# Performance work log

Measured on AMD Instinct MI355X. Metric: run time of the kernel, lower is better.

Reference implementation:

```python
import jax, jax.numpy as jnp
import numpy as np

K = 16  # memory_topk

def signed_abs_softmax(x, axis=-1):
    # sign(x) * softmax(|x|): the module's 'signed_abs_softmax' route/edge compression
    return jnp.sign(x) * jax.nn.softmax(jnp.abs(x), axis=axis)

def unit_norm(v, eps=1e-6):
    return v / (jnp.linalg.norm(v, axis=-1, keepdims=True) + eps)

def setup_inputs() -> dict:
    key = jax.random.key(0)
    ks = jax.random.split(key, 7)
    B, T, D, S, R = 8, 2048, 512, 2048, 64
    std = 0.02
    return {
        "x": jax.random.normal(ks[0], (B, T, D), jnp.float32),
        "init_state": std * jax.random.normal(ks[1], (S,), jnp.float32),
        "init_val": std * jax.random.normal(ks[2], (S, D), jnp.float32),
        "route_a": std * jax.random.normal(ks[3], (D, R), jnp.float32),
        "route_b": std * jax.random.normal(ks[4], (R, S), jnp.float32),
        "pair_a": std * jax.random.normal(ks[5], (D, R), jnp.float32),
        "pair_b": std * jax.random.normal(ks[6], (D, R), jnp.float32),
    }

def reference(x, init_state, init_val, route_a, route_b, pair_a, pair_b):
    B, T, D = x.shape
    S = init_val.shape[0]
    b_idx = jnp.arange(B)[:, None, None]

    # --- initialize memory level (signed-softmax state, unit-norm values) ---
    state = jnp.broadcast_to(signed_abs_softmax(init_state), (B, S))
    val = jnp.broadcast_to(unit_norm(init_val), (B, S, D))

    # --- SparseTransition write: topk route tokens -> slots, scatter-add ---
    scores = jnp.einsum('btd,dr,rs->bts', x, route_a, route_b)   # [B,T,S] low-rank route
    _, idx = jax.lax.top_k(jnp.abs(scores), K)                    # [B,T,K] topk by magnitude
    g = jnp.take_along_axis(scores, idx, axis=-1)                 # signed gathered scores
    w = signed_abs_softmax(g, axis=-1)                            # route compression
    v = unit_norm(x)                                              # use_direction_only=True
    val_delta = jnp.zeros((B, S, D), x.dtype).at[b_idx, idx].add(w[..., None] * v[:, :, None, :])
    state_delta = jnp.zeros((B, S), x.dtype).at[b_idx, idx].add(jax.nn.softplus(g))
    state = signed_abs_softmax(state + state_delta, axis=-1)      # merge='add' + signed softmax state
    val = unit_norm(val + val_delta)                              # merge='add' + unit-norm values

    # --- SparsePropagation: topk pairwise edges among slots, residual mix ---
    q = jnp.einsum('bsd,dr->bsr', val, pair_a)
    kk = jnp.einsum('bsd,dr->bsr', val, pair_b)
    p = jnp.einsum('bir,bjr->bij', q, kk)                         # [B,S,S] low-rank pairwise
    _, eidx = jax.lax.top_k(jnp.abs(p), K)                        # [B,S,K] topk edges per slot
    pe = jnp.take_along_axis(p, eidx, axis=-1)
    ew = signed_abs_softmax(pe, axis=-1)                          # edge compression
    nbr = val[b_idx, eidx]                                        # [B,S,K,D] gather neighbor values
    delta = jnp.einsum('bsk,bskd->bsd', ew, nbr)
    val = unit_norm(val + delta)                                  # residual + unit-norm

    # pack (state, val) into one array: [B,S,1+D]
    return jnp.concatenate([state[..., None], val], axis=-1)
```

## Files before the change

### kernel.cpp

```cpp
#include <hip/hip_runtime.h>
#include <cmath>

namespace {
constexpr int B = 8;
constexpr int T = 2048;
constexpr int D = 512;
constexpr int S = 2048;
constexpr int R = 64;
constexpr int KTOP = 16;
constexpr int NT = 8;
constexpr int NR = 16;
constexpr int NI = 8;
constexpr int CAP = 256;

__device__ __forceinline__ float signf(float v) {
    return (v > 0.f) ? 1.f : ((v < 0.f) ? -1.f : 0.f);
}

__device__ __forceinline__ void topk16_row(float* __restrict__ row,
                                           unsigned long long* __restrict__ cand,
                                           int lane, float& myg, int& myj) {
    const float4* p4 = (const float4*)row;
    float lmax = 0.f;
#pragma unroll
    for (int i = 0; i < 8; i++) {
        float4 v = p4[lane + 64 * i];
        lmax = fmaxf(lmax, fmaxf(fmaxf(fabsf(v.x), fabsf(v.y)),
                                 fmaxf(fabsf(v.z), fabsf(v.w))));
    }
    {
        float v = lmax;
#pragma unroll
        for (int size = 2; size <= 64; size <<= 1) {
#pragma unroll
            for (int stride = size >> 1; stride > 0; stride >>= 1) {
                float o = __shfl_xor(v, stride, 64);
                bool takeMax = ((lane & size) == 0) == ((lane & stride) == 0);
                v = takeMax ? fmaxf(v, o) : fminf(v, o);
            }
        }
        lmax = __shfl(v, 15);
    }
    float t = lmax;
    int cnt = 0;
#pragma unroll
    for (int i = 0; i < 8; i++) {
        float4 v = p4[lane + 64 * i];
        cnt += (fabsf(v.x) >= t) + (fabsf(v.y) >= t) +
               (fabsf(v.z) >= t) + (fabsf(v.w) >= t);
    }
    int off = cnt;
#pragma unroll
    for (int d = 1; d < 64; d <<= 1) {
        int o = __shfl_up(off, d, 64);
        if (lane >= d) off += o;
    }
    int total = __shfl(off, 63);
    int base = off - cnt;

    if (total <= 64) {
        int pos = base;
#pragma unroll
        for (int i = 0; i < 8; i++) {
            float4 v = p4[lane + 64 * i];
            int jb = 4 * (lane + 64 * i);
            float c[4] = {v.x, v.y, v.z, v.w};
#pragma unroll
            for (int cc = 0; cc < 4; cc++) {
                if (fabsf(c[cc]) >= t) {
                    unsigned ab = __float_as_uint(c[cc]) & 0x7fffffffu;
                    cand[pos++] = ((unsigned long long)ab << 11) |
                                  (unsigned)(2047 - (jb + cc));
                }
            }
        }
        unsigned long long key = (lane < total) ? cand[lane] : 0ull;
#pragma unroll
        for (int size = 2; size <= 64; size <<= 1) {
#pragma unroll
            for (int stride = size >> 1; stride > 0; stride >>= 1) {
                unsigned long long o = __shfl_xor((long long)key, stride, 64);
                bool takeMax = ((lane & size) == 0) == ((lane & stride) == 0);
                key = (takeMax == (key > o)) ? key : o;
            }
        }
        myg = 0.f; myj = 0;
        if (lane < KTOP) {
            myj = 2047 - (int)(key & 2047ull);
            myg = row[myj];
        }
    } else {
        myg = 0.f; myj = 0;
        for (int k = 0; k < KTOP; k++) {
            float bv = -1.f, bs = 0.f; int bj = 0;
#pragma unroll
            for (int i = 0; i < 8; i++) {
                float4 v = p4[lane + 64 * i];
                int jb = 4 * (lane + 64 * i);
                { float a = fabsf(v.x); if (a > bv) { bv = a; bs = v.x; bj = jb; } }
                { float a = fabsf(v.y); if (a > bv) { bv = a; bs = v.y; bj = jb + 1; } }
                { float a = fabsf(v.z); if (a > bv) { bv = a; bs = v.z; bj = jb + 2; } }
                { float a = fabsf(v.w); if (a > bv) { bv = a; bs = v.w; bj = jb + 3; } }
            }
#pragma unroll
            for (int off2 = 32; off2 > 0; off2 >>= 1) {
                float ov = __shfl_xor(bv, off2, 64);
                float os = __shfl_xor(bs, off2, 64);
                int   oj = __shfl_xor(bj, off2, 64);
                if (ov > bv || (ov == bv && oj < bj)) { bv = ov; bs = os; bj = oj; }
            }
            if (lane == k) { myg = bs; myj = bj; }
            if (lane == 0) row[bj] = 0.f;
        }
    }
}
}

__global__ void k_init_state(const float* __restrict__ init_state,
                             float* __restrict__ state_ws) {
    int b = blockIdx.x;
    int tid = threadIdx.x;
    __shared__ float red[256];
    float m = -1e30f;
    for (int s = tid; s < S; s += 256) m = fmaxf(m, fabsf(init_state[s]));
    red[tid] = m; __syncthreads();
    for (int off = 128; off > 0; off >>= 1) {
        if (tid < off) red[tid] = fmaxf(red[tid], red[tid + off]);
        __syncthreads();
    }
    m = red[0]; __syncthreads();
    float sum = 0.f;
    for (int s = tid; s < S; s += 256) sum += expf(fabsf(init_state[s]) - m);
    red[tid] = sum; __syncthreads();
    for (int off = 128; off > 0; off >>= 1) {
        if (tid < off) red[tid] += red[tid + off];
        __syncthreads();
    }
    float inv = 1.0f / red[0];
    for (int s = tid; s < S; s += 256) {
        float v = init_state[s];
        state_ws[(size_t)b * S + s] = signf(v) * expf(fabsf(v) - m) * inv;
    }
}

__global__ void k_bcast(const float* __restrict__ init_val,
                        float* __restrict__ val1) {
    int wv = threadIdx.x >> 6;
    int lane = threadIdx.x & 63;
    int blk = ((blockIdx.x & 7) << 9) | (blockIdx.x >> 3);
    int row = blk * 4 + wv;
    int s = row & (S - 1);
    const float4* src = (const float4*)(init_val + (size_t)s * D);
    float4 v0 = src[lane], v1 = src[lane + 64];
    float ss = v0.x * v0.x + v0.y * v0.y + v0.z * v0.z + v0.w * v0.w
             + v1.x * v1.x + v1.y * v1.y + v1.z * v1.z + v1.w * v1.w;
#pragma unroll
    for (int off = 32; off > 0; off >>= 1) ss += __shfl_xor(ss, off, 64);
    float sc = 1.0f / (sqrtf(ss) + 1e-6f);
    v0.x *= sc; v0.y *= sc; v0.z *= sc; v0.w *= sc;
    v1.x *= sc; v1.y *= sc; v1.z *= sc; v1.w *= sc;
    float4* dst = (float4*)(val1 + (size_t)row * D);
    dst[lane] = v0; dst[lane + 64] = v1;
}

__global__ void __launch_bounds__(512, 4) k_score(const float* __restrict__ x,
                                                  const float* __restrict__ route_a,
                                                  const float* __restrict__ route_b,
                                                  float* __restrict__ val1,
                                                  float* __restrict__ state_ws,
                                                  float* __restrict__ coef,
                                                  int* __restrict__ bincount,
                                                  int* __restrict__ binlist) {
    __shared__ __align__(16) char smem[NT * S * 4];
    __shared__ __align__(16) float xr[NT][R];
    __shared__ unsigned long long cand[NT][64];
    float (*sc)[S] = (float(*)[S])smem;
    float (*xs)[D] = (float(*)[D])smem;
    float (*red4)[512] = (float(*)[512])smem;

    int tid = threadIdx.x;
    int lane = tid & 63, wv = tid >> 6;
    int blk = ((blockIdx.x & 7) << 8) | (blockIdx.x >> 3);
    int tb = blk * NT;
    int b = tb >> 11;
    int t0 = tb & (T - 1);

    {
        const float4* xg = (const float4*)(x + (size_t)tb * D);
        float4* xls = (float4*)smem;
        xls[tid] = xg[tid];
        xls[tid + 512] = xg[tid + 512];
    }
    __syncthreads();

    {
        int r = lane;
        float acc[NT];
#pragma unroll
        for (int tt = 0; tt < NT; tt++) acc[tt] = 0.f;
        for (int d0 = wv * 64; d0 < wv * 64 + 64; d0 += 4) {
            float a0 = route_a[(size_t)(d0 + 0) * R + r];
            float a1 = route_a[(size_t)(d0 + 1) * R + r];
            float a2 = route_a[(size_t)(d0 + 2) * R + r];
            float a3 = route_a[(size_t)(d0 + 3) * R + r];
#pragma unroll
            for (int tt = 0; tt < NT; tt++) {
                float4 xv = *(const float4*)&xs[tt][d0];
                acc[tt] += xv.x * a0 + xv.y * a1 + xv.z * a2 + xv.w * a3;
            }
        }
        __syncthreads();
#pragma unroll
        for (int tt = 0; tt < NT; tt++) red4[tt][tid] = acc[tt];
        __syncthreads();
        {
            int tt2 = tid >> 6, r2 = tid & 63;
            float s = 0.f;
#pragma unroll
            for (int g = 0; g < 8; g++) s += red4[tt2][g * 64 + r2];
            xr[tt2][r2] = s;
        }
        __syncthreads();
    }

    {
        const float4* rb4 = (const float4*)route_b;
        int j4 = tid;
        float4 acc[NT];
#pragma unroll
        for (int tt = 0; tt < NT; tt++) acc[tt] = make_float4(0.f, 0.f, 0.f, 0.f);
        for (int r0 = 0; r0 < R; r0 += 4) {
            float4 xv[NT];
#pragma unroll
            for (int tt = 0; tt < NT; tt++) xv[tt] = *(const float4*)&xr[tt][r0];
#define SCORE_STEP(dr, comp)                                                   \
            {                                                                  \
                float4 bv = rb4[(size_t)(r0 + dr) * (S / 4) + j4];             \
                _Pragma("unroll")                                              \
                for (int tt = 0; tt < NT; tt++) {                              \
                    float c = xv[tt].comp;                                     \
                    acc[tt].x += c * bv.x; acc[tt].y += c * bv.y;              \
                    acc[tt].z += c * bv.z; acc[tt].w += c * bv.w;              \
                }                                                              \
            }
            SCORE_STEP(0, x) SCORE_STEP(1, y) SCORE_STEP(2, z) SCORE_STEP(3, w)
#undef SCORE_STEP
        }
#pragma unroll
        for (int tt = 0; tt < NT; tt++)
            ((float4*)&sc[tt][0])[j4] = acc[tt];
    }
    __syncthreads();

    int tt = wv;
    int tloc = t0 + tt;
    int tglob = tb + tt;

    float xinv;
    {
        const float4* xg = (const float4*)(x + (size_t)tglob * D);
        float4 x0 = xg[lane], x1 = xg[lane + 64];
        float ss = x0.x * x0.x + x0.y * x0.y + x0.z * x0.z + x0.w * x0.w
                 + x1.x * x1.x + x1.y * x1.y + x1.z * x1.z + x1.w * x1.w;
#pragma unroll
        for (int off = 32; off > 0; off >>= 1) ss += __shfl_xor(ss, off, 64);
        xinv = 1.0f / (sqrtf(ss) + 1e-6f);
    }

    float myg; int myj;
    topk16_row(&sc[tt][0], &cand[wv][0], lane, myg, myj);

    float m = __shfl(fabsf(myg), 0);
    float e = (lane < KTOP) ? expf(fabsf(myg) - m) : 0.f;
    float esum = e;
#pragma unroll
    for (int off = 8; off > 0; off >>= 1) esum += __shfl_xor(esum, off, 64);
    esum = __shfl(esum, 0);
    float w = signf(myg) * e / esum;
    float coefv = w * xinv;

    unsigned long long ovf = 0ull;
    int pos = 0;
    if (lane < KTOP) {
        float sp = (myg > 20.f) ? myg : log1pf(expf(myg));
        atomicAdd(&state_ws[(size_t)b * S + myj], sp);
        pos = atomicAdd(&bincount[(size_t)b * S + myj], 1);
        if (pos < CAP) {
            binlist[((size_t)b * S + myj) * CAP + pos] = (tloc << 4) | lane;
            coef[(size_t)tglob * KTOP + lane] = coefv;
        }
    }
    ovf = __ballot(lane < KTOP && pos >= CAP);
    while (ovf) {
        int src = __ffsll(ovf) - 1;
        int j = __shfl(myj, src);
        float c = __shfl(coefv, src);
        float* dst = val1 + ((size_t)b * S + j) * D;
        const float* xrow = x + (size_t)tglob * D;
#pragma unroll
        for (int i = 0; i < 8; i++)
            atomicAdd(&dst[lane + 64 * i], c * xrow[lane + 64 * i]);
        ovf &= ovf - 1;
    }
}

__global__ void __launch_bounds__(256) k_accum(const float* __restrict__ x,
                                               const float* __restrict__ coef,
                                               const int* __restrict__ bincount,
                                               const int* __restrict__ binlist,
                                               float* __restrict__ val1) {
    int lane = threadIdx.x & 63, wv = threadIdx.x >> 6;
    int blk = ((blockIdx.x & 7) << 9) | (blockIdx.x >> 3);
    int row = blk * 4 + wv;
    int b = row >> 11;
    float4* vp4 = (float4*)(val1 + (size_t)row * D);
    float4 a0 = vp4[lane], a1 = vp4[lane + 64];
    int n = bincount[row]; if (n > CAP) n = CAP;
    const int* lp = binlist + (size_t)row * CAP;
    for (int base = 0; base < n; base += 64) {
        int mm = n - base; if (mm > 64) mm = 64;
        int ent = 0; float cc = 0.f;
        if (lane < mm) {
            ent = lp[base + lane];
            cc = coef[((size_t)b * T + (ent >> 4)) * KTOP + (ent & 15)];
        }
        int e0 = __shfl(ent, 0);
        const float4* xp4 = (const float4*)(x + ((size_t)b * T + (e0 >> 4)) * D);
        float4 v0 = xp4[lane], v1 = xp4[lane + 64];
        for (int k = 0; k < mm; k++) {
            float c = __shfl(cc, k);
            float4 c0 = v0, c1 = v1;
            if (k + 1 < mm) {
                int e2 = __shfl(ent, k + 1);
                const float4* np4 = (const float4*)(x + ((size_t)b * T + (e2 >> 4)) * D);
                v0 = np4[lane]; v1 = np4[lane + 64];
            }
            a0.x += c * c0.x; a0.y += c * c0.y; a0.z += c * c0.z; a0.w += c * c0.w;
            a1.x += c * c1.x; a1.y += c * c1.y; a1.z += c * c1.z; a1.w += c * c1.w;
        }
    }
    float ss = a0.x * a0.x + a0.y * a0.y + a0.z * a0.z + a0.w * a0.w
             + a1.x * a1.x + a1.y * a1.y + a1.z * a1.z + a1.w * a1.w;
#pragma unroll
    for (int off = 32; off > 0; off >>= 1) ss += __shfl_xor(ss, off, 64);
    float sc = 1.0f / (sqrtf(ss) + 1e-6f);
    a0.x *= sc; a0.y *= sc; a0.z *= sc; a0.w *= sc;
    a1.x *= sc; a1.y *= sc; a1.z *= sc; a1.w *= sc;
    vp4[lane] = a0; vp4[lane + 64] = a1;
}

__global__ void k_state_final(const float* __restrict__ state_ws,
                              float* __restrict__ out) {
    int b = blockIdx.x;
    int tid = threadIdx.x;
    __shared__ float red[256];
    const float* sp = state_ws + (size_t)b * S;
    float m = -1e30f;
    for (int s = tid; s < S; s += 256) m = fmaxf(m, fabsf(sp[s]));
    red[tid] = m; __syncthreads();
    for (int off = 128; off > 0; off >>= 1) {
        if (tid < off) red[tid] = fmaxf(red[tid], red[tid + off]);
        __syncthreads();
    }
    m = red[0]; __syncthreads();
    float sum = 0.f;
    for (int s = tid; s < S; s += 256) sum += expf(fabsf(sp[s]) - m);
    red[tid] = sum; __syncthreads();
    for (int off = 128; off > 0; off >>= 1) {
        if (tid < off) red[tid] += red[tid + off];
        __syncthreads();
    }
    float inv = 1.0f / red[0];
    for (int s = tid; s < S; s += 256) {
        float v = sp[s];
        out[((size_t)b * S + s) * (D + 1)] = signf(v) * expf(fabsf(v) - m) * inv;
    }
}

__global__ void __launch_bounds__(256) k_qk(const float* __restrict__ val1,
                                            const float* __restrict__ pair_a,
                                            const float* __restrict__ pair_b,
                                            float* __restrict__ q,
                                            float* __restrict__ kkT) {
    __shared__ __align__(16) float vrow[NR][D];
    __shared__ float redq[256];
    __shared__ float redk[256];
    int tid = threadIdx.x;
    int blk = ((blockIdx.x & 7) << 7) | (blockIdx.x >> 3);
    int rowbase = blk * NR;
    int b = rowbase >> 11;
    int sbase = rowbase & (S - 1);
    {
        const float4* gv = (const float4*)(val1 + (size_t)rowbase * D);
        float4* lv = (float4*)&vrow[0][0];
        for (int i = tid; i < NR * D / 4; i += 256) lv[i] = gv[i];
    }
    __syncthreads();
    int r = tid & 63, grp = tid >> 6;
    float accq[NR], acck[NR];
#pragma unroll
    for (int rr = 0; rr < NR; rr++) { accq[rr] = 0.f; acck[rr] = 0.f; }
    for (int d0 = grp * 128; d0 < grp * 128 + 128; d0 += 4) {
#pragma unroll
        for (int dd = 0; dd < 4; dd++) {
            float a  = pair_a[(size_t)(d0 + dd) * R + r];
            float bb = pair_b[(size_t)(d0 + dd) * R + r];
#pragma unroll
            for (int rr = 0; rr < NR; rr++) {
                float v = vrow[rr][d0 + dd];
                accq[rr] += v * a;
                acck[rr] += v * bb;
            }
        }
    }
    for (int rr = 0; rr < NR; rr++) {
        redq[tid] = accq[rr]; redk[tid] = acck[rr];
        __syncthreads();
        if (tid < 64) {
            float qv = redq[tid] + redq[tid + 64] + redq[tid + 128] + redq[tid + 192];
            float kv = redk[tid] + redk[tid + 64] + redk[tid + 128] + redk[tid + 192];
            q[(size_t)(rowbase + rr) * R + tid] = qv;
            kkT[((size_t)b * R + tid) * S + (sbase + rr)] = kv;
        }
        __syncthreads();
    }
}

__global__ void __launch_bounds__(512) k_pscore(const float* __restrict__ q,
                                                const float* __restrict__ kkT,
                                                int* __restrict__ eidx,
                                                float* __restrict__ ew_g) {
    __shared__ __align__(16) float prow[NI][S];
    __shared__ __align__(16) float qrow[NI][R];
    __shared__ unsigned long long cand[NI][64];

    int tid = threadIdx.x;
    int lane = tid & 63, wv = tid >> 6;
    int blk = ((blockIdx.x & 7) << 8) | (blockIdx.x >> 3);
    int ibase = blk * NI;
    int b = ibase >> 11;

    {
        int rr = tid >> 6, r = tid & 63;
        qrow[rr][r] = q[(size_t)(ibase + rr) * R + r];
    }
    __syncthreads();

    {
        const float4* kk4 = (const float4*)(kkT + (size_t)b * R * S);
        int j4 = tid;
        float4 acc[NI];
#pragma unroll
        for (int rr = 0; rr < NI; rr++) acc[rr] = make_float4(0.f, 0.f, 0.f, 0.f);
        for (int r0 = 0; r0 < R; r0 += 4) {
            float4 qv[NI];
#pragma unroll
            for (int rr = 0; rr < NI; rr++) qv[rr] = *(const float4*)&qrow[rr][r0];
#define P_STEP(dr, comp)                                                       \
            {                                                                  \
                float4 kv = kk4[(size_t)(r0 + dr) * (S / 4) + j4];             \
                _Pragma("unroll")                                              \
                for (int rr = 0; rr < NI; rr++) {                              \
                    float c = qv[rr].comp;                                     \
                    acc[rr].x += c * kv.x; acc[rr].y += c * kv.y;              \
                    acc[rr].z += c * kv.z; acc[rr].w += c * kv.w;              \
                }                                                              \
            }
            P_STEP(0, x) P_STEP(1, y) P_STEP(2, z) P_STEP(3, w)
#undef P_STEP
        }
#pragma unroll
        for (int rr = 0; rr < NI; rr++)
            ((float4*)&prow[rr][0])[j4] = acc[rr];
    }
    __syncthreads();

    int row = ibase + wv;
    float myg; int myj;
    topk16_row(&prow[wv][0], &cand[wv][0], lane, myg, myj);

    float m = __shfl(fabsf(myg), 0);
    float e = (lane < KTOP) ? expf(fabsf(myg) - m) : 0.f;
    float esum = e;
#pragma unroll
    for (int off = 8; off > 0; off >>= 1) esum += __shfl_xor(esum, off, 64);
    esum = __shfl(esum, 0);
    float myw = signf(myg) * e / esum;

    if (lane < KTOP) {
        eidx[(size_t)row * KTOP + lane] = myj;
        ew_g[(size_t)row * KTOP + lane] = myw;
    }
}

__global__ void __launch_bounds__(256) k_mix(const int* __restrict__ eidx,
                                             const float* __restrict__ ew_g,
                                             const float* __restrict__ val1,
                                             float* __restrict__ out) {
    int lane = threadIdx.x & 63, wv = threadIdx.x >> 6;
    int blk = ((blockIdx.x & 7) << 9) | (blockIdx.x >> 3);
    int row = blk * 4 + wv;
    int b = row >> 11;

    int e_i = 0; float e_w = 0.f;
    if (lane < KTOP) {
        e_i = eidx[(size_t)row * KTOP + lane];
        e_w = ew_g[(size_t)row * KTOP + lane];
    }

    const float4* self4 = (const float4*)(val1 + (size_t)row * D);
    float4 a0 = self4[lane], a1 = self4[lane + 64];
#pragma unroll
    for (int k = 0; k < KTOP; k++) {
        int j = __shfl(e_i, k);
        float w = __shfl(e_w, k);
        const float4* nb4 = (const float4*)(val1 + ((size_t)b * S + j) * D);
        float4 v0 = nb4[lane], v1 = nb4[lane + 64];
        a0.x += w * v0.x; a0.y += w * v0.y; a0.z += w * v0.z; a0.w += w * v0.w;
        a1.x += w * v1.x; a1.y += w * v1.y; a1.z += w * v1.z; a1.w += w * v1.w;
    }
    float ss = a0.x * a0.x + a0.y * a0.y + a0.z * a0.z + a0.w * a0.w
             + a1.x * a1.x + a1.y * a1.y + a1.z * a1.z + a1.w * a1.w;
#pragma unroll
    for (int off = 32; off > 0; off >>= 1) ss += __shfl_xor(ss, off, 64);
    float sc = 1.0f / (sqrtf(ss) + 1e-6f);
    float* op = out + (size_t)row * (D + 1) + 1;
    int d0 = 4 * lane;
    op[d0 + 0] = a0.x * sc; op[d0 + 1] = a0.y * sc;
    op[d0 + 2] = a0.z * sc; op[d0 + 3] = a0.w * sc;
    op[256 + d0 + 0] = a1.x * sc; op[256 + d0 + 1] = a1.y * sc;
    op[256 + d0 + 2] = a1.z * sc; op[256 + d0 + 3] = a1.w * sc;
}

extern "C" void kernel_launch(void* const* d_in, const int* in_sizes, int n_in,
                              void* d_out, int out_size, void* d_ws, size_t ws_size,
                              hipStream_t stream) {
    (void)in_sizes; (void)n_in; (void)out_size; (void)ws_size;
    const float* x          = (const float*)d_in[0];
    const float* init_state = (const float*)d_in[1];
    const float* init_val   = (const float*)d_in[2];
    const float* route_a    = (const float*)d_in[3];
    const float* route_b    = (const float*)d_in[4];
    const float* pair_a     = (const float*)d_in[5];
    const float* pair_b     = (const float*)d_in[6];
    float* out = (float*)d_out;

    float* ws       = (float*)d_ws;
    float* val1     = ws;
    float* q        = val1 + (size_t)B * S * D;
    float* kkT      = q    + (size_t)B * S * R;
    float* state_ws = kkT  + (size_t)B * R * S;
    float* coef     = state_ws + (size_t)B * S;
    int*   bincount = (int*)(coef + (size_t)B * T * KTOP);
    int*   binlist  = bincount + (size_t)B * S;
    int*   eidx     = binlist;
    float* ew       = (float*)(binlist + (size_t)B * S * KTOP);

    hipMemsetAsync(bincount, 0, (size_t)B * S * sizeof(int), stream);
    hipLaunchKernelGGL(k_init_state, dim3(B), dim3(256), 0, stream, init_state, state_ws);
    hipLaunchKernelGGL(k_bcast, dim3(B * S / 4), dim3(256), 0, stream, init_val, val1);
    hipLaunchKernelGGL(k_score, dim3(B * T / NT), dim3(512), 0, stream,
                       x, route_a, route_b, val1, state_ws, coef, bincount, binlist);
    hipLaunchKernelGGL(k_state_final, dim3(B), dim3(256), 0, stream, state_ws, out);
    hipLaunchKernelGGL(k_accum, dim3(B * S / 4), dim3(256), 0, stream,
                       x, coef, bincount, binlist, val1);
    hipLaunchKernelGGL(k_qk, dim3(B * S / NR), dim3(256), 0, stream,
                       val1, pair_a, pair_b, q, kkT);
    hipLaunchKernelGGL(k_pscore, dim3(B * S / NI), dim3(512), 0, stream,
                       q, kkT, eidx, ew);
    hipLaunchKernelGGL(k_mix, dim3(B * S / 4), dim3(256), 0, stream,
                       eidx, ew, val1, out);
}
```

Baseline: 413.1 us.

## Fuse init broadcast into accumulate, defer state softmax, replace overflow atomics with list

Removes the separate init-state and broadcast kernels. The normalized init_val is now computed inside k_accum, so the full B*S*D val1 initialization write and read go away. State softmax is split into a single-block reduction kernel plus a per-row finalization in k_mix. Overflow bins no longer do atomic adds into val1; they are appended to a global overflow list that every k_accum wave scans linearly, which could be costly if there are many overflows. The x norm now reads from LDS instead of global memory.

```diff
diff --git a/kernel.cpp b/kernel.cpp
--- a/kernel.cpp
+++ b/kernel.cpp
@@ -12,6 +12,7 @@
 constexpr int NR = 16;
 constexpr int NI = 8;
 constexpr int CAP = 256;
+constexpr int OVFCAP = 32768;
 
 __device__ __forceinline__ float signf(float v) {
     return (v > 0.f) ? 1.f : ((v < 0.f) ? -1.f : 0.f);
@@ -116,61 +117,16 @@
 }
 }
 
-__global__ void k_init_state(const float* __restrict__ init_state,
-                             float* __restrict__ state_ws) {
-    int b = blockIdx.x;
-    int tid = threadIdx.x;
-    __shared__ float red[256];
-    float m = -1e30f;
-    for (int s = tid; s < S; s += 256) m = fmaxf(m, fabsf(init_state[s]));
-    red[tid] = m; __syncthreads();
-    for (int off = 128; off > 0; off >>= 1) {
-        if (tid < off) red[tid] = fmaxf(red[tid], red[tid + off]);
-        __syncthreads();
-    }
-    m = red[0]; __syncthreads();
-    float sum = 0.f;
-    for (int s = tid; s < S; s += 256) sum += expf(fabsf(init_state[s]) - m);
-    red[tid] = sum; __syncthreads();
-    for (int off = 128; off > 0; off >>= 1) {
-        if (tid < off) red[tid] += red[tid + off];
-        __syncthreads();
-    }
-    float inv = 1.0f / red[0];
-    for (int s = tid; s < S; s += 256) {
-        float v = init_state[s];
-        state_ws[(size_t)b * S + s] = signf(v) * expf(fabsf(v) - m) * inv;
-    }
-}
-
-__global__ void k_bcast(const float* __restrict__ init_val,
-                        float* __restrict__ val1) {
-    int wv = threadIdx.x >> 6;
-    int lane = threadIdx.x & 63;
-    int blk = ((blockIdx.x & 7) << 9) | (blockIdx.x >> 3);
-    int row = blk * 4 + wv;
-    int s = row & (S - 1);
-    const float4* src = (const float4*)(init_val + (size_t)s * D);
-    float4 v0 = src[lane], v1 = src[lane + 64];
-    float ss = v0.x * v0.x + v0.y * v0.y + v0.z * v0.z + v0.w * v0.w
-             + v1.x * v1.x + v1.y * v1.y + v1.z * v1.z + v1.w * v1.w;
-#pragma unroll
-    for (int off = 32; off > 0; off >>= 1) ss += __shfl_xor(ss, off, 64);
-    float sc = 1.0f / (sqrtf(ss) + 1e-6f);
-    v0.x *= sc; v0.y *= sc; v0.z *= sc; v0.w *= sc;
-    v1.x *= sc; v1.y *= sc; v1.z *= sc; v1.w *= sc;
-    float4* dst = (float4*)(val1 + (size_t)row * D);
-    dst[lane] = v0; dst[lane + 64] = v1;
-}
-
 __global__ void __launch_bounds__(512, 4) k_score(const float* __restrict__ x,
                                                   const float* __restrict__ route_a,
                                                   const float* __restrict__ route_b,
-                                                  float* __restrict__ val1,
                                                   float* __restrict__ state_ws,
                                                   float* __restrict__ coef,
                                                   int* __restrict__ bincount,
-                                                  int* __restrict__ binlist) {
+                                                  int* __restrict__ binlist,
+                                                  int* __restrict__ ovf_cnt,
+                                                  int* __restrict__ ovf_key,
+                                                  float* __restrict__ ovf_c) {
     __shared__ __align__(16) char smem[NT * S * 4];
     __shared__ __align__(16) float xr[NT][R];
     __shared__ unsigned long long cand[NT][64];
@@ -192,6 +148,17 @@
         xls[tid + 512] = xg[tid + 512];
     }
     __syncthreads();
+
+    float xinv;
+    {
+        const float4* xst = (const float4*)&xs[wv][0];
+        float4 x0 = xst[lane], x1 = xst[lane + 64];
+        float ssx = x0.x * x0.x + x0.y * x0.y + x0.z * x0.z + x0.w * x0.w
+                  + x1.x * x1.x + x1.y * x1.y + x1.z * x1.z + x1.w * x1.w;
+#pragma unroll
+        for (int off = 32; off > 0; off >>= 1) ssx += __shfl_xor(ssx, off, 64);
+        xinv = 1.0f / (sqrtf(ssx) + 1e-6f);
+    }
 
     {
         int r = lane;
@@ -256,17 +223,6 @@
     int tloc = t0 + tt;
     int tglob = tb + tt;
 
-    float xinv;
-    {
-        const float4* xg = (const float4*)(x + (size_t)tglob * D);
-        float4 x0 = xg[lane], x1 = xg[lane + 64];
-        float ss = x0.x * x0.x + x0.y * x0.y + x0.z * x0.z + x0.w * x0.w
-                 + x1.x * x1.x + x1.y * x1.y + x1.z * x1.z + x1.w * x1.w;
-#pragma unroll
-        for (int off = 32; off > 0; off >>= 1) ss += __shfl_xor(ss, off, 64);
-        xinv = 1.0f / (sqrtf(ss) + 1e-6f);
-    }
-
     float myg; int myj;
     topk16_row(&sc[tt][0], &cand[wv][0], lane, myg, myj);
 
@@ -279,42 +235,50 @@
     float w = signf(myg) * e / esum;
     float coefv = w * xinv;
 
-    unsigned long long ovf = 0ull;
-    int pos = 0;
     if (lane < KTOP) {
         float sp = (myg > 20.f) ? myg : log1pf(expf(myg));
         atomicAdd(&state_ws[(size_t)b * S + myj], sp);
-        pos = atomicAdd(&bincount[(size_t)b * S + myj], 1);
+        int pos = atomicAdd(&bincount[(size_t)b * S + myj], 1);
         if (pos < CAP) {
             binlist[((size_t)b * S + myj) * CAP + pos] = (tloc << 4) | lane;
             coef[(size_t)tglob * KTOP + lane] = coefv;
-        }
-    }
-    ovf = __ballot(lane < KTOP && pos >= CAP);
-    while (ovf) {
-        int src = __ffsll(ovf) - 1;
-        int j = __shfl(myj, src);
-        float c = __shfl(coefv, src);
-        float* dst = val1 + ((size_t)b * S + j) * D;
-        const float* xrow = x + (size_t)tglob * D;
-#pragma unroll
-        for (int i = 0; i < 8; i++)
-            atomicAdd(&dst[lane + 64 * i], c * xrow[lane + 64 * i]);
-        ovf &= ovf - 1;
+        } else {
+            int i = atomicAdd(ovf_cnt, 1);
+            if (i < OVFCAP) {
+                ovf_key[i] = ((b * S + myj) << 11) | tloc;
+                ovf_c[i] = coefv;
+            }
+        }
     }
 }
 
 __global__ void __launch_bounds__(256) k_accum(const float* __restrict__ x,
+                                               const float* __restrict__ init_val,
                                                const float* __restrict__ coef,
                                                const int* __restrict__ bincount,
                                                const int* __restrict__ binlist,
+                                               const int* __restrict__ ovf_cnt,
+                                               const int* __restrict__ ovf_key,
+                                               const float* __restrict__ ovf_c,
                                                float* __restrict__ val1) {
     int lane = threadIdx.x & 63, wv = threadIdx.x >> 6;
     int blk = ((blockIdx.x & 7) << 9) | (blockIdx.x >> 3);
     int row = blk * 4 + wv;
     int b = row >> 11;
-    float4* vp4 = (float4*)(val1 + (size_t)row * D);
-    float4 a0 = vp4[lane], a1 = vp4[lane + 64];
+    int s_idx = row & (S - 1);
+
+    const float4* src = (const float4*)(init_val + (size_t)s_idx * D);
+    float4 a0 = src[lane], a1 = src[lane + 64];
+    {
+        float ss0 = a0.x * a0.x + a0.y * a0.y + a0.z * a0.z + a0.w * a0.w
+                  + a1.x * a1.x + a1.y * a1.y + a1.z * a1.z + a1.w * a1.w;
+#pragma unroll
+        for (int off = 32; off > 0; off >>= 1) ss0 += __shfl_xor(ss0, off, 64);
+        float bsc = 1.0f / (sqrtf(ss0) + 1e-6f);
+        a0.x *= bsc; a0.y *= bsc; a0.z *= bsc; a0.w *= bsc;
+        a1.x *= bsc; a1.y *= bsc; a1.z *= bsc; a1.w *= bsc;
+    }
+
     int n = bincount[row]; if (n > CAP) n = CAP;
     const int* lp = binlist + (size_t)row * CAP;
     for (int base = 0; base < n; base += 64) {
@@ -339,6 +303,20 @@
             a1.x += c * c1.x; a1.y += c * c1.y; a1.z += c * c1.z; a1.w += c * c1.w;
         }
     }
+
+    int oc = *ovf_cnt; if (oc > OVFCAP) oc = OVFCAP;
+    for (int i = 0; i < oc; i++) {
+        int key = ovf_key[i];
+        if ((key >> 11) == row) {
+            float c = ovf_c[i];
+            int tg = ((row >> 11) << 11) | (key & 2047);
+            const float4* xp4 = (const float4*)(x + (size_t)tg * D);
+            float4 v0 = xp4[lane], v1 = xp4[lane + 64];
+            a0.x += c * v0.x; a0.y += c * v0.y; a0.z += c * v0.z; a0.w += c * v0.w;
+            a1.x += c * v1.x; a1.y += c * v1.y; a1.z += c * v1.z; a1.w += c * v1.w;
+        }
+    }
+
     float ss = a0.x * a0.x + a0.y * a0.y + a0.z * a0.z + a0.w * a0.w
              + a1.x * a1.x + a1.y * a1.y + a1.z * a1.z + a1.w * a1.w;
 #pragma unroll
@@ -346,35 +324,72 @@
     float sc = 1.0f / (sqrtf(ss) + 1e-6f);
     a0.x *= sc; a0.y *= sc; a0.z *= sc; a0.w *= sc;
     a1.x *= sc; a1.y *= sc; a1.z *= sc; a1.w *= sc;
+    float4* vp4 = (float4*)(val1 + (size_t)row * D);
     vp4[lane] = a0; vp4[lane + 64] = a1;
 }
 
-__global__ void k_state_final(const float* __restrict__ state_ws,
-                              float* __restrict__ out) {
-    int b = blockIdx.x;
-    int tid = threadIdx.x;
-    __shared__ float red[256];
-    const float* sp = state_ws + (size_t)b * S;
-    float m = -1e30f;
-    for (int s = tid; s < S; s += 256) m = fmaxf(m, fabsf(sp[s]));
-    red[tid] = m; __syncthreads();
-    for (int off = 128; off > 0; off >>= 1) {
-        if (tid < off) red[tid] = fmaxf(red[tid], red[tid + off]);
-        __syncthreads();
-    }
-    m = red[0]; __syncthreads();
+__global__ void __launch_bounds__(512) k_state_red(const float* __restrict__ init_state,
+                                                   const float* __restrict__ state_ws,
+                                                   float* base_ws,
+                                                   float* sm_m, float* sm_inv) {
+    __shared__ float red[16];
+    __shared__ float base_lds[S];
+    int tid = threadIdx.x, lane = tid & 63, wv = tid >> 6;
+
+    float4 v = ((const float4*)init_state)[tid];
+    float m = fmaxf(fmaxf(fabsf(v.x), fabsf(v.y)), fmaxf(fabsf(v.z), fabsf(v.w)));
+#pragma unroll
+    for (int off = 32; off > 0; off >>= 1) m = fmaxf(m, __shfl_xor(m, off, 64));
+    if (lane == 0) red[wv] = m;
+    __syncthreads();
+    float M = red[0];
+#pragma unroll
+    for (int i = 1; i < 8; i++) M = fmaxf(M, red[i]);
+    __syncthreads();
+    float s = expf(fabsf(v.x) - M) + expf(fabsf(v.y) - M) +
+              expf(fabsf(v.z) - M) + expf(fabsf(v.w) - M);
+#pragma unroll
+    for (int off = 32; off > 0; off >>= 1) s += __shfl_xor(s, off, 64);
+    if (lane == 0) red[wv] = s;
+    __syncthreads();
+    float SUM = 0.f;
+#pragma unroll
+    for (int i = 0; i < 8; i++) SUM += red[i];
+    float inv = 1.0f / SUM;
+    float4 bo;
+    bo.x = signf(v.x) * expf(fabsf(v.x) - M) * inv;
+    bo.y = signf(v.y) * expf(fabsf(v.y) - M) * inv;
+    bo.z = signf(v.z) * expf(fabsf(v.z) - M) * inv;
+    bo.w = signf(v.w) * expf(fabsf(v.w) - M) * inv;
+    ((float4*)base_ws)[tid] = bo;
+    ((float4*)base_lds)[tid] = bo;
+    __syncthreads();
+
+    int b = wv;
+    const float4* dp = (const float4*)(state_ws + (size_t)b * S);
+    const float4* bp = (const float4*)base_lds;
+    float4 c[8];
+    float vm = 0.f;
+#pragma unroll
+    for (int i = 0; i < 8; i++) {
+        float4 dv = dp[lane + 64 * i];
+        float4 bv = bp[lane + 64 * i];
+        c[i].x = bv.x + dv.x; c[i].y = bv.y + dv.y;
+        c[i].z = bv.z + dv.z; c[i].w = bv.w + dv.w;
+        vm = fmaxf(vm, fmaxf(fmaxf(fabsf(c[i].x), fabsf(c[i].y)),
+                             fmaxf(fabsf(c[i].z), fabsf(c[i].w))));
+    }
+#pragma unroll
+    for (int off = 32; off > 0; off >>= 1) vm = fmaxf(vm, __shfl_xor(vm, off, 64));
     float sum = 0.f;
-    for (int s = tid; s < S; s += 256) sum += expf(fabsf(sp[s]) - m);
-    red[tid] = sum; __syncthreads();
-    for (int off = 128; off > 0; off >>= 1) {
-        if (tid < off) red[tid] += red[tid + off];
-        __syncthreads();
-    }
-    float inv = 1.0f / red[0];
-    for (int s = tid; s < S; s += 256) {
-        float v = sp[s];
-        out[((size_t)b * S + s) * (D + 1)] = signf(v) * expf(fabsf(v) - m) * inv;
-    }
+#pragma unroll
+    for (int i = 0; i < 8; i++) {
+        sum += expf(fabsf(c[i].x) - vm) + expf(fabsf(c[i].y) - vm) +
+               expf(fabsf(c[i].z) - vm) + expf(fabsf(c[i].w) - vm);
+    }
+#pragma unroll
+    for (int off = 32; off > 0; off >>= 1) sum += __shfl_xor(sum, off, 64);
+    if (lane == 0) { sm_m[b] = vm; sm_inv[b] = 1.0f / sum; }
 }
 
 __global__ void __launch_bounds__(256) k_qk(const float* __restrict__ val1,
@@ -496,6 +511,10 @@
 __global__ void __launch_bounds__(256) k_mix(const int* __restrict__ eidx,
                                              const float* __restrict__ ew_g,
                                              const float* __restrict__ val1,
+                                             const float* __restrict__ base_ws,
+                                             const float* __restrict__ state_ws,
+                                             const float* __restrict__ sm_m,
+                                             const float* __restrict__ sm_inv,
                                              float* __restrict__ out) {
     int lane = threadIdx.x & 63, wv = threadIdx.x >> 6;
     int blk = ((blockIdx.x & 7) << 9) | (blockIdx.x >> 3);
@@ -530,6 +549,12 @@
     op[d0 + 2] = a0.z * sc; op[d0 + 3] = a0.w * sc;
     op[256 + d0 + 0] = a1.x * sc; op[256 + d0 + 1] = a1.y * sc;
     op[256 + d0 + 2] = a1.z * sc; op[256 + d0 + 3] = a1.w * sc;
+
+    if (lane == 0) {
+        float vv = base_ws[row & (S - 1)] + state_ws[row];
+        out[(size_t)row * (D + 1)] =
+            signf(vv) * expf(fabsf(vv) - sm_m[b]) * sm_inv[b];
+    }
 }
 
 extern "C" void kernel_launch(void* const* d_in, const int* in_sizes, int n_in,
@@ -549,25 +574,32 @@
     float* val1     = ws;
     float* q        = val1 + (size_t)B * S * D;
     float* kkT      = q    + (size_t)B * S * R;
-    float* state_ws = kkT  + (size_t)B * R * S;
-    float* coef     = state_ws + (size_t)B * S;
-    int*   bincount = (int*)(coef + (size_t)B * T * KTOP);
-    int*   binlist  = bincount + (size_t)B * S;
+    float* coef     = kkT  + (size_t)B * R * S;
+    int*   binlist  = (int*)(coef + (size_t)B * T * KTOP);
+    float* state_ws = (float*)(binlist + (size_t)B * S * CAP);
+    int*   bincount = (int*)(state_ws + (size_t)B * S);
+    int*   ovf_cnt  = bincount + (size_t)B * S;
+    int*   ovf_key  = ovf_cnt + 16;
+    float* ovf_c    = (float*)(ovf_key + OVFCAP);
+    float* base_ws  = ovf_c + OVFCAP;
+    float* sm_m     = base_ws + S;
+    float* sm_inv   = sm_m + B;
     int*   eidx     = binlist;
     float* ew       = (float*)(binlist + (size_t)B * S * KTOP);
 
-    hipMemsetAsync(bincount, 0, (size_t)B * S * sizeof(int), stream);
-    hipLaunchKernelGGL(k_init_state, dim3(B), dim3(256), 0, stream, init_state, state_ws);
-    hipLaunchKernelGGL(k_bcast, dim3(B * S / 4), dim3(256), 0, stream, init_val, val1);
+    hipMemsetAsync(state_ws, 0, (size_t)(2 * B * S + 16) * sizeof(int), stream);
     hipLaunchKernelGGL(k_score, dim3(B * T / NT), dim3(512), 0, stream,
-                       x, route_a, route_b, val1, state_ws, coef, bincount, binlist);
-    hipLaunchKernelGGL(k_state_final, dim3(B), dim3(256), 0, stream, state_ws, out);
+                       x, route_a, route_b, state_ws, coef, bincount, binlist,
+                       ovf_cnt, ovf_key, ovf_c);
+    hipLaunchKernelGGL(k_state_red, dim3(1), dim3(512), 0, stream,
+                       init_state, state_ws, base_ws, sm_m, sm_inv);
     hipLaunchKernelGGL(k_accum, dim3(B * S / 4), dim3(256), 0, stream,
-                       x, coef, bincount, binlist, val1);
+                       x, init_val, coef, bincount, binlist,
+                       ovf_cnt, ovf_key, ovf_c, val1);
     hipLaunchKernelGGL(k_qk, dim3(B * S / NR), dim3(256), 0, stream,
                        val1, pair_a, pair_b, q, kkT);
     hipLaunchKernelGGL(k_pscore, dim3(B * S / NI), dim3(512), 0, stream,
                        q, kkT, eidx, ew);
     hipLaunchKernelGGL(k_mix, dim3(B * S / 4), dim3(256), 0, stream,
-                       eidx, ew, val1, out);
-}
+                       eidx, ew, val1, base_ws, state_ws, sm_m, sm_inv, out);
+}
```

New measurement: 410.9 us. No clear change (-0.5%).
